# Kernel optimization log

Measured on AMD Instinct MI355X. Metric: run time of the kernel, lower is better.

## Reference

```python
import jax, jax.numpy as jnp
import numpy as np

TAU = 2.0      # LIFNode default tau
V_TH = 1.0     # default v_threshold
ALPHA = 4.0    # surrogate.Sigmoid default alpha

@jax.custom_vjp
def spike_fn(x):
    # heaviside: spike if membrane potential crosses threshold
    return (x >= 0.0).astype(x.dtype)

def _spike_fwd(x):
    return spike_fn(x), x

def _spike_bwd(x, g):
    s = jax.nn.sigmoid(ALPHA * x)
    return (g * ALPHA * s * (1.0 - s),)

spike_fn.defvjp(_spike_fwd, _spike_bwd)

def lif_step(v, inp):
    # decay_input=True, v_reset=0.0 (hard reset):
    # v <- v + (inp - v)/tau ; spike = H(v - v_th) ; v <- v*(1-spike)
    v = v + (inp - v) / TAU
    s = spike_fn(v - V_TH)
    v = v * (1.0 - s)
    return v, s

def setup_inputs() -> dict:
    key = jax.random.key(0)
    k_x, k1, k2, k3 = jax.random.split(key, 4)
    T, B, H, W = 16, 64, 150, 400
    x = jax.random.normal(k_x, (T, B, H, W), dtype=jnp.float32)
    # torch Linear default init: U(-1/sqrt(fan_in), 1/sqrt(fan_in))
    def lin_init(k, out_f, in_f):
        bound = 1.0 / np.sqrt(in_f)
        return jax.random.uniform(k, (out_f, in_f), dtype=jnp.float32,
                                  minval=-bound, maxval=bound)
    W1 = lin_init(k1, 200, 60000)
    W2 = lin_init(k2, 50, 200)
    W3 = lin_init(k3, 2, 50)
    return {"x": x, "W1": W1, "W2": W2, "W3": W3}

def reference(x, W1, W2, W3):
    T, B = x.shape[0], x.shape[1]
    xf = x.reshape(T, B, -1)  # layer.Flatten over non-(T,B) dims -> [T,B,60000]
    D1, D2, D3 = W1.shape[0], W2.shape[0], W3.shape[0]

    def step(carry, xt):
        v1, v2, v3 = carry
        h1 = xt @ W1.T            # [B,200]
        v1, s1 = lif_step(v1, h1)
        h2 = s1 @ W2.T            # [B,50]
        v2, s2 = lif_step(v2, h2)
        h3 = s2 @ W3.T            # [B,2]
        v3, s3 = lif_step(v3, h3)
        return (v1, v2, v3), s3

    init = (jnp.zeros((B, D1), x.dtype),
            jnp.zeros((B, D2), x.dtype),
            jnp.zeros((B, D3), x.dtype))
    _, out = jax.lax.scan(step, init, xf)  # out: [T,B,2] spike trains
    return out
```

## Files before the change

### kernel.cpp

```cpp
#include <hip/hip_runtime.h>
#include <hip/hip_bf16.h>

#define T_STEPS 16
#define BATCH   64
#define M_ROWS  1024
#define K_DIM   60000
#define N1      200
#define N2      50
#define N3      2
#define HN      (M_ROWS * N1)
#define BK      32

typedef __attribute__((ext_vector_type(8)))  short bf16x8;
typedef __attribute__((ext_vector_type(16))) float f32x16;

static __device__ __forceinline__ bf16x8 cvt8(float4 lo, float4 hi) {
    union { bf16x8 v; __hip_bfloat162 h[4]; } u;
    u.h[0] = __float22bfloat162_rn(make_float2(lo.x, lo.y));
    u.h[1] = __float22bfloat162_rn(make_float2(lo.z, lo.w));
    u.h[2] = __float22bfloat162_rn(make_float2(hi.x, hi.y));
    u.h[3] = __float22bfloat162_rn(make_float2(hi.z, hi.w));
    return u.v;
}

static __device__ __forceinline__ float bf2f(unsigned short u) {
    unsigned int x = (unsigned int)u << 16;
    return __uint_as_float(x);
}

static __device__ __forceinline__ void lgkm_barrier() {
    __builtin_amdgcn_sched_barrier(0);
    asm volatile("s_waitcnt lgkmcnt(0)\n\ts_barrier" ::: "memory");
    __builtin_amdgcn_sched_barrier(0);
}

template <int KSEG, int KSTEPS, int NWG>
__global__ __launch_bounds__(512, 4)
void gemm_lds(const float* __restrict__ x,
              const float* __restrict__ w1,
              unsigned short* __restrict__ part) {
    __shared__ __align__(16) char smem[2][24576];

    const int tid = threadIdx.x;
    const int l   = tid & 63;
    const int wv  = tid >> 6;
    const int wm  = wv & 1;
    const int wn  = wv >> 1;

    const int hw      = blockIdx.y * 8 + blockIdx.x;
    const int logical = (hw & 7) * (NWG / 8) + (hw >> 3);
    const int s  = logical >> 3;
    const int mt = logical & 7;

    const int m0 = mt * 128;
    const int k0 = s * KSEG;

    const int ar = tid >> 2;
    const int ag = tid & 3;
    const float* asrc = x + (size_t)(m0 + ar) * K_DIM + k0 + ag * 8;
    const int aw_off = ar * 64 + ((ag ^ ((ar >> 1) & 3)) << 4);

    const int br = tid >> 1;
    const int bh = tid & 1;
    const bool bvalid = br < N1;
    const float* bsrc = w1 + (size_t)br * K_DIM + k0 + bh * 16;
    const int bg0 = bh * 2;
    const int bw_off0 = 8192 + br * 64 + (((bg0)     ^ ((br >> 1) & 3)) << 4);
    const int bw_off1 = 8192 + br * 64 + (((bg0 + 1) ^ ((br >> 1) & 3)) << 4);

    f32x16 acc[2][2];
    #pragma unroll
    for (int i = 0; i < 2; ++i)
        #pragma unroll
        for (int j = 0; j < 2; ++j)
            #pragma unroll
            for (int q = 0; q < 16; ++q) acc[i][j][q] = 0.f;

    float4 pA[2][2];
    float4 pB[4];

    {
        float4 a0 = *(const float4*)asrc;
        float4 a1 = *(const float4*)(asrc + 4);
        float4 b0, b1, b2, b3;
        if (bvalid) {
            b0 = *(const float4*)bsrc;
            b1 = *(const float4*)(bsrc + 4);
            b2 = *(const float4*)(bsrc + 8);
            b3 = *(const float4*)(bsrc + 12);
        }
        pA[1][0] = *(const float4*)(asrc + BK);
        pA[1][1] = *(const float4*)(asrc + BK + 4);
        if (bvalid) {
            const float* bp = bsrc + BK;
            pB[0] = *(const float4*)bp;
            pB[1] = *(const float4*)(bp + 4);
            pB[2] = *(const float4*)(bp + 8);
            pB[3] = *(const float4*)(bp + 12);
        }
        *(bf16x8*)(smem[0] + aw_off) = cvt8(a0, a1);
        if (bvalid) {
            *(bf16x8*)(smem[0] + bw_off0) = cvt8(b0, b1);
            *(bf16x8*)(smem[0] + bw_off1) = cvt8(b2, b3);
        }
    }
    lgkm_barrier();

    const int fr = l & 31;
    const int fh = (l >> 5) * 16;

    #pragma unroll
    for (int it = 0; it < KSTEPS; ++it) {
        const int cur = it & 1;
        const bool more = (it + 1) < KSTEPS;

        if (more) {
            const int jn = (it + 2 < KSTEPS) ? (it + 2) : (KSTEPS - 1);
            pA[cur][0] = *(const float4*)(asrc + jn * BK);
            pA[cur][1] = *(const float4*)(asrc + jn * BK + 4);
        }
        __builtin_amdgcn_sched_barrier(0);

        const char* ab = smem[cur];
        const char* bb = smem[cur] + 8192;
        #pragma unroll
        for (int kk = 0; kk < 2; ++kk) {
            const int r0 = wm * 64 + fr;
            const int r1 = wm * 64 + 32 + fr;
            bf16x8 a0 = *(const bf16x8*)(ab + r0 * 64 + ((kk * 32 + fh) ^ (((r0 >> 1) & 3) << 4)));
            bf16x8 a1 = *(const bf16x8*)(ab + r1 * 64 + ((kk * 32 + fh) ^ (((r1 >> 1) & 3) << 4)));
            #pragma unroll
            for (int fn = 0; fn < 2; ++fn) {
                if (wn == 3 && fn == 1) continue;
                const int n = wn * 64 + fn * 32 + fr;
                bf16x8 bv = *(const bf16x8*)(bb + n * 64 + ((kk * 32 + fh) ^ (((n >> 1) & 3) << 4)));
                acc[0][fn] = __builtin_amdgcn_mfma_f32_32x32x16_bf16(a0, bv, acc[0][fn], 0, 0, 0);
                acc[1][fn] = __builtin_amdgcn_mfma_f32_32x32x16_bf16(a1, bv, acc[1][fn], 0, 0, 0);
            }
        }
        __builtin_amdgcn_sched_barrier(0);

        if (more) {
            char* nb = smem[cur ^ 1];
            *(bf16x8*)(nb + aw_off) = cvt8(pA[cur ^ 1][0], pA[cur ^ 1][1]);
            if (bvalid) {
                *(bf16x8*)(nb + bw_off0) = cvt8(pB[0], pB[1]);
                *(bf16x8*)(nb + bw_off1) = cvt8(pB[2], pB[3]);
                if ((it + 2) < KSTEPS) {
                    const float* bp = bsrc + (size_t)(it + 2) * BK;
                    pB[0] = *(const float4*)bp;
                    pB[1] = *(const float4*)(bp + 4);
                    pB[2] = *(const float4*)(bp + 8);
                    pB[3] = *(const float4*)(bp + 12);
                }
            }
            lgkm_barrier();
        }
    }

    const int col = l & 31;
    const int rhi = (l >> 5) * 4;
    #pragma unroll
    for (int fm = 0; fm < 2; ++fm)
        #pragma unroll
        for (int fn = 0; fn < 2; ++fn) {
            const int gn = wn * 64 + fn * 32 + col;
            if (gn < N1) {
                const int gmb = m0 + wm * 64 + fm * 32 + rhi;
                #pragma unroll
                for (int r = 0; r < 16; ++r) {
                    const int gm = gmb + (r & 3) + 8 * (r >> 2);
                    __hip_bfloat16 hv = __float2bfloat16(acc[fm][fn][r]);
                    part[(size_t)s * HN + (size_t)gm * N1 + gn] = *(unsigned short*)&hv;
                }
            }
        }
}

template <int KSPLIT>
__global__ __launch_bounds__(256)
void reduce_kernel(const unsigned short* __restrict__ part, float* __restrict__ h1) {
    const size_t f = ((size_t)blockIdx.x * 256 + threadIdx.x) * 2;
    float a0 = 0.f, a1 = 0.f;
    #pragma unroll 25
    for (int s = 0; s < KSPLIT; ++s) {
        const unsigned int v = *(const unsigned int*)(part + (size_t)s * HN + f);
        a0 += bf2f((unsigned short)(v & 0xFFFFu));
        a1 += bf2f((unsigned short)(v >> 16));
    }
    h1[f]     = a0;
    h1[f + 1] = a1;
}

__global__ __launch_bounds__(256)
void tail_kernel(const float* __restrict__ h1,
                 const float* __restrict__ w2, const float* __restrict__ w3,
                 float* __restrict__ out) {
    __shared__ float w2s[N2 * N1];
    __shared__ float w3s[N3 * N2];
    __shared__ unsigned long long msk[T_STEPS][4];

    const int b    = blockIdx.x;
    const int i    = threadIdx.x;
    const int wv   = i >> 6;
    const int lane = i & 63;

    for (int o = i; o < (N2 * N1) / 4; o += 256)
        ((float4*)w2s)[o] = ((const float4*)w2)[o];
    if (i < N3 * N2) w3s[i] = w3[i];

    float h[T_STEPS];
    #pragma unroll
    for (int t = 0; t < T_STEPS; ++t)
        h[t] = (i < N1) ? h1[(size_t)(t * BATCH + b) * N1 + i] : 0.f;

    float v1 = 0.f;
    #pragma unroll
    for (int t = 0; t < T_STEPS; ++t) {
        v1 += (h[t] - v1) * 0.5f;
        bool sp = (v1 - 1.0f) >= 0.f;
        unsigned long long m = __ballot(sp);
        if (sp) v1 = 0.f;
        if (lane == 0) msk[t][wv] = m;
    }
    __syncthreads();

    if (wv == 0) {
        float v2 = 0.f, v3 = 0.f;
        for (int t = 0; t < T_STEPS; ++t) {
            float h2 = 0.f;
            if (lane < N2) {
                #pragma unroll
                for (int w = 0; w < 4; ++w) {
                    unsigned long long m = msk[t][w];
                    while (m) {
                        int lz = __builtin_ctzll(m);
                        m &= m - 1;
                        h2 += w2s[lane * N1 + (w * 64 + lz)];
                    }
                }
            }
            v2 += (h2 - v2) * 0.5f;
            bool sp2 = (v2 - 1.0f) >= 0.f;
            unsigned long long bal2 = __ballot(sp2);
            if (sp2) v2 = 0.f;

            float h3 = 0.f;
            if (lane < N3) {
                unsigned long long m = bal2;
                while (m) {
                    int j = __builtin_ctzll(m);
                    m &= m - 1;
                    h3 += w3s[lane * N2 + j];
                }
            }
            v3 += (h3 - v3) * 0.5f;
            bool sp3 = (v3 - 1.0f) >= 0.f;
            if (lane < N3)
                out[(size_t)(t * BATCH + b) * N3 + lane] = sp3 ? 1.f : 0.f;
            if (sp3) v3 = 0.f;
        }
    }
}

extern "C" void kernel_launch(void* const* d_in, const int* in_sizes, int n_in,
                              void* d_out, int out_size, void* d_ws, size_t ws_size,
                              hipStream_t stream) {
    const float* x  = (const float*)d_in[0];
    const float* w1 = (const float*)d_in[1];
    const float* w2 = (const float*)d_in[2];
    const float* w3 = (const float*)d_in[3];
    float* out = (float*)d_out;

    const size_t h1_bytes  = (size_t)HN * 4;
    const size_t need125 = (size_t)125 * HN * 2 + h1_bytes;
    const bool big = ws_size >= need125;

    const int ksplit = big ? 125 : 25;
    unsigned short* part = (unsigned short*)d_ws;
    float* h1 = (float*)((char*)d_ws + (size_t)ksplit * HN * 2);

    if (big) {
        dim3 g(8, 125);
        gemm_lds<480, 15, 1000><<<g, 512, 0, stream>>>(x, w1, part);
        reduce_kernel<125><<<HN / 512, 256, 0, stream>>>(part, h1);
    } else {
        dim3 g(8, 25);
        gemm_lds<2400, 75, 200><<<g, 512, 0, stream>>>(x, w1, part);
        reduce_kernel<25><<<HN / 512, 256, 0, stream>>>(part, h1);
    }
    tail_kernel<<<BATCH, 256, 0, stream>>>(h1, w2, w3, out);
}
```

Measured before the change: 99.94 us.

## Split N dimension into two 128-wide tiles to double workgroup count

Each GEMM workgroup now covers 128 rows by 128 columns of the 200-wide output instead of all 256 padded columns. This doubles the grid, halves the LDS per block and the accumulator registers, and raises the occupancy hint from 4 to 6. Waves whose columns fall entirely past 200 skip their MFMA work. The cost is that x (the A operand) is now read from global memory and converted twice, once per N tile, which doubles the dominant input traffic, and the second tile wastes 56 of its 128 columns.

```diff
diff --git a/kernel.cpp b/kernel.cpp
--- a/kernel.cpp
+++ b/kernel.cpp
@@ -35,11 +35,11 @@
 }
 
 template <int KSEG, int KSTEPS, int NWG>
-__global__ __launch_bounds__(512, 4)
+__global__ __launch_bounds__(512, 6)
 void gemm_lds(const float* __restrict__ x,
               const float* __restrict__ w1,
               unsigned short* __restrict__ part) {
-    __shared__ __align__(16) char smem[2][24576];
+    __shared__ __align__(16) char smem[2][16384];
 
     const int tid = threadIdx.x;
     const int l   = tid & 63;
@@ -47,12 +47,15 @@
     const int wm  = wv & 1;
     const int wn  = wv >> 1;
 
-    const int hw      = blockIdx.y * 8 + blockIdx.x;
+    const int hw      = blockIdx.y * 16 + blockIdx.x;
     const int logical = (hw & 7) * (NWG / 8) + (hw >> 3);
-    const int s  = logical >> 3;
-    const int mt = logical & 7;
+    const int s    = logical >> 4;
+    const int mtnt = logical & 15;
+    const int mt   = mtnt >> 1;
+    const int nt   = mtnt & 1;
 
     const int m0 = mt * 128;
+    const int n0 = nt * 128;
     const int k0 = s * KSEG;
 
     const int ar = tid >> 2;
@@ -60,49 +63,41 @@
     const float* asrc = x + (size_t)(m0 + ar) * K_DIM + k0 + ag * 8;
     const int aw_off = ar * 64 + ((ag ^ ((ar >> 1) & 3)) << 4);
 
-    const int br = tid >> 1;
-    const int bh = tid & 1;
-    const bool bvalid = br < N1;
-    const float* bsrc = w1 + (size_t)br * K_DIM + k0 + bh * 16;
-    const int bg0 = bh * 2;
-    const int bw_off0 = 8192 + br * 64 + (((bg0)     ^ ((br >> 1) & 3)) << 4);
-    const int bw_off1 = 8192 + br * 64 + (((bg0 + 1) ^ ((br >> 1) & 3)) << 4);
-
-    f32x16 acc[2][2];
+    const int br = tid >> 2;
+    const int bg = tid & 3;
+    const int grow = n0 + br;
+    const bool bvalid = grow < N1;
+    const float* bsrc = w1 + (size_t)grow * K_DIM + k0 + bg * 8;
+    const int bw_off = 8192 + br * 64 + ((bg ^ ((br >> 1) & 3)) << 4);
+
+    const bool wactive = (n0 + wn * 32) < N1;
+
+    f32x16 acc[2];
     #pragma unroll
     for (int i = 0; i < 2; ++i)
         #pragma unroll
-        for (int j = 0; j < 2; ++j)
-            #pragma unroll
-            for (int q = 0; q < 16; ++q) acc[i][j][q] = 0.f;
+        for (int q = 0; q < 16; ++q) acc[i][q] = 0.f;
 
     float4 pA[2][2];
-    float4 pB[4];
+    float4 pB[2];
 
     {
         float4 a0 = *(const float4*)asrc;
         float4 a1 = *(const float4*)(asrc + 4);
-        float4 b0, b1, b2, b3;
+        float4 b0, b1;
         if (bvalid) {
             b0 = *(const float4*)bsrc;
             b1 = *(const float4*)(bsrc + 4);
-            b2 = *(const float4*)(bsrc + 8);
-            b3 = *(const float4*)(bsrc + 12);
         }
         pA[1][0] = *(const float4*)(asrc + BK);
         pA[1][1] = *(const float4*)(asrc + BK + 4);
         if (bvalid) {
-            const float* bp = bsrc + BK;
-            pB[0] = *(const float4*)bp;
-            pB[1] = *(const float4*)(bp + 4);
-            pB[2] = *(const float4*)(bp + 8);
-            pB[3] = *(const float4*)(bp + 12);
+            pB[0] = *(const float4*)(bsrc + BK);
+            pB[1] = *(const float4*)(bsrc + BK + 4);
         }
         *(bf16x8*)(smem[0] + aw_off) = cvt8(a0, a1);
-        if (bvalid) {
-            *(bf16x8*)(smem[0] + bw_off0) = cvt8(b0, b1);
-            *(bf16x8*)(smem[0] + bw_off1) = cvt8(b2, b3);
-        }
+        if (bvalid)
+            *(bf16x8*)(smem[0] + bw_off) = cvt8(b0, b1);
     }
     lgkm_barrier();
 
@@ -121,21 +116,19 @@
         }
         __builtin_amdgcn_sched_barrier(0);
 
-        const char* ab = smem[cur];
-        const char* bb = smem[cur] + 8192;
-        #pragma unroll
-        for (int kk = 0; kk < 2; ++kk) {
-            const int r0 = wm * 64 + fr;
-            const int r1 = wm * 64 + 32 + fr;
-            bf16x8 a0 = *(const bf16x8*)(ab + r0 * 64 + ((kk * 32 + fh) ^ (((r0 >> 1) & 3) << 4)));
-            bf16x8 a1 = *(const bf16x8*)(ab + r1 * 64 + ((kk * 32 + fh) ^ (((r1 >> 1) & 3) << 4)));
+        if (wactive) {
+            const char* ab = smem[cur];
+            const char* bb = smem[cur] + 8192;
             #pragma unroll
-            for (int fn = 0; fn < 2; ++fn) {
-                if (wn == 3 && fn == 1) continue;
-                const int n = wn * 64 + fn * 32 + fr;
+            for (int kk = 0; kk < 2; ++kk) {
+                const int r0 = wm * 64 + fr;
+                const int r1 = wm * 64 + 32 + fr;
+                const int n  = wn * 32 + fr;
+                bf16x8 a0 = *(const bf16x8*)(ab + r0 * 64 + ((kk * 32 + fh) ^ (((r0 >> 1) & 3) << 4)));
+                bf16x8 a1 = *(const bf16x8*)(ab + r1 * 64 + ((kk * 32 + fh) ^ (((r1 >> 1) & 3) << 4)));
                 bf16x8 bv = *(const bf16x8*)(bb + n * 64 + ((kk * 32 + fh) ^ (((n >> 1) & 3) << 4)));
-                acc[0][fn] = __builtin_amdgcn_mfma_f32_32x32x16_bf16(a0, bv, acc[0][fn], 0, 0, 0);
-                acc[1][fn] = __builtin_amdgcn_mfma_f32_32x32x16_bf16(a1, bv, acc[1][fn], 0, 0, 0);
+                acc[0] = __builtin_amdgcn_mfma_f32_32x32x16_bf16(a0, bv, acc[0], 0, 0, 0);
+                acc[1] = __builtin_amdgcn_mfma_f32_32x32x16_bf16(a1, bv, acc[1], 0, 0, 0);
             }
         }
         __builtin_amdgcn_sched_barrier(0);
@@ -144,14 +137,11 @@
             char* nb = smem[cur ^ 1];
             *(bf16x8*)(nb + aw_off) = cvt8(pA[cur ^ 1][0], pA[cur ^ 1][1]);
             if (bvalid) {
-                *(bf16x8*)(nb + bw_off0) = cvt8(pB[0], pB[1]);
-                *(bf16x8*)(nb + bw_off1) = cvt8(pB[2], pB[3]);
+                *(bf16x8*)(nb + bw_off) = cvt8(pB[0], pB[1]);
                 if ((it + 2) < KSTEPS) {
                     const float* bp = bsrc + (size_t)(it + 2) * BK;
                     pB[0] = *(const float4*)bp;
                     pB[1] = *(const float4*)(bp + 4);
-                    pB[2] = *(const float4*)(bp + 8);
-                    pB[3] = *(const float4*)(bp + 12);
                 }
             }
             lgkm_barrier();
@@ -160,21 +150,19 @@
 
     const int col = l & 31;
     const int rhi = (l >> 5) * 4;
-    #pragma unroll
-    for (int fm = 0; fm < 2; ++fm)
+    const int gn  = n0 + wn * 32 + col;
+    if (gn < N1) {
         #pragma unroll
-        for (int fn = 0; fn < 2; ++fn) {
-            const int gn = wn * 64 + fn * 32 + col;
-            if (gn < N1) {
-                const int gmb = m0 + wm * 64 + fm * 32 + rhi;
-                #pragma unroll
-                for (int r = 0; r < 16; ++r) {
-                    const int gm = gmb + (r & 3) + 8 * (r >> 2);
-                    __hip_bfloat16 hv = __float2bfloat16(acc[fm][fn][r]);
-                    part[(size_t)s * HN + (size_t)gm * N1 + gn] = *(unsigned short*)&hv;
-                }
-            }
-        }
+        for (int fm = 0; fm < 2; ++fm) {
+            const int gmb = m0 + wm * 64 + fm * 32 + rhi;
+            #pragma unroll
+            for (int r = 0; r < 16; ++r) {
+                const int gm = gmb + (r & 3) + 8 * (r >> 2);
+                __hip_bfloat16 hv = __float2bfloat16(acc[fm][r]);
+                part[(size_t)s * HN + (size_t)gm * N1 + gn] = *(unsigned short*)&hv;
+            }
+        }
+    }
 }
 
 template <int KSPLIT>
@@ -281,12 +269,12 @@
     float* h1 = (float*)((char*)d_ws + (size_t)ksplit * HN * 2);
 
     if (big) {
-        dim3 g(8, 125);
-        gemm_lds<480, 15, 1000><<<g, 512, 0, stream>>>(x, w1, part);
+        dim3 g(16, 125);
+        gemm_lds<480, 15, 2000><<<g, 512, 0, stream>>>(x, w1, part);
         reduce_kernel<125><<<HN / 512, 256, 0, stream>>>(part, h1);
     } else {
-        dim3 g(8, 25);
-        gemm_lds<2400, 75, 200><<<g, 512, 0, stream>>>(x, w1, part);
+        dim3 g(16, 25);
+        gemm_lds<2400, 75, 400><<<g, 512, 0, stream>>>(x, w1, part);
         reduce_kernel<25><<<HN / 512, 256, 0, stream>>>(part, h1);
     }
     tail_kernel<<<BATCH, 256, 0, stream>>>(h1, w2, w3, out);
```

New measurement: 105.4 us. +5.5%, slower.
